# Kernel optimization log

Hardware: AMD Instinct MI355X
Metric: run time of the kernel (lower is better)

## Reference

```python
import jax, jax.numpy as jnp
import numpy as np

N_USER = 100000
N_ITEM = 50000
N = N_USER + N_ITEM  # 150000 nodes
D = 64               # embedding_size
L = 3                # num_layers
E = 2000000          # edges
B = 8192             # batch of (user, item_p, item_n) triples
INT_W, POP_W, TIDE_W = 0.1, 0.1, 0.2


def setup_inputs() -> dict:
    key = jax.random.key(0)
    ks = jax.random.split(key, 10)
    stdv = 1.0 / np.sqrt(D)
    emb_int = jax.random.uniform(ks[0], (N, D), minval=-stdv, maxval=stdv, dtype=jnp.float32)
    emb_pop = jax.random.uniform(ks[1], (N, D), minval=-stdv, maxval=stdv, dtype=jnp.float32)
    q = jax.random.uniform(ks[2], (N_ITEM,), dtype=jnp.float32)
    b = jax.random.uniform(ks[3], (N_ITEM,), dtype=jnp.float32)
    user = jax.random.randint(ks[4], (B, 1), 0, N_USER)
    item_p = jax.random.randint(ks[5], (B, 1), 0, N_ITEM)
    item_n = jax.random.randint(ks[6], (B, 1), 0, N_ITEM)
    mask = jax.random.randint(ks[7], (B, 1), 0, 2).astype(bool)
    edge_src = jax.random.randint(ks[8], (E,), 0, N)
    edge_dst = jax.random.randint(ks[9], (E,), 0, N)
    return {"emb_int": emb_int, "emb_pop": emb_pop, "q": q, "b": b,
            "user": user, "item_p": item_p, "item_n": item_n, "mask": mask,
            "edge_src": edge_src, "edge_dst": edge_dst}


def reference(emb_int, emb_pop, q, b, user, item_p, item_n, mask, edge_src, edge_dst):
    # --- LightGCN symmetric normalization coefficients (per edge) ---
    ones = jnp.ones(edge_src.shape, emb_int.dtype)
    deg_out = jax.ops.segment_sum(ones, edge_src, num_segments=N)
    deg_in = jax.ops.segment_sum(ones, edge_dst, num_segments=N)
    norm = (jax.lax.rsqrt(jnp.maximum(deg_out, 1.0))[edge_src]
            * jax.lax.rsqrt(jnp.maximum(deg_in, 1.0))[edge_dst])  # [E]

    def propagate(e0):
        # L layers of LGConv (gather-scale-scatter), mean over layer outputs incl. layer 0.
        # Dropout is identity in eval mode (training=False).
        acc, h = e0, e0
        for _ in range(L):
            h = jax.ops.segment_sum(h[edge_src] * norm[:, None], edge_dst, num_segments=N)
            acc = acc + h
        return acc / (L + 1)

    f_int = propagate(emb_int)  # [N, D]
    f_pop = propagate(emb_pop)  # [N, D]

    ip = item_p + N_USER  # item node ids
    inn = item_n + N_USER
    u_i, u_p = f_int[user], f_pop[user]          # [B, 1, D]
    pi_i, pi_p = f_int[ip], f_pop[ip]
    ni_i, ni_p = f_int[inn], f_pop[inn]

    p_score_int = jnp.sum(u_i * pi_i, axis=2)    # [B, 1]
    n_score_int = jnp.sum(u_i * ni_i, axis=2)
    p_score_pop = jnp.sum(u_p * pi_p, axis=2)
    n_score_pop = jnp.sum(u_p * ni_p, axis=2)
    p_score_total = p_score_int + p_score_pop
    n_score_total = n_score_int + n_score_pop

    mf = mask.astype(p_score_int.dtype)
    nmf = (~mask).astype(p_score_int.dtype)

    def mask_bpr(p, n, m):
        return -jnp.mean(m * jax.nn.log_sigmoid(p - n))

    def bpr(p, n):
        return -jnp.mean(jax.nn.log_sigmoid(p - n))

    loss_int = mask_bpr(p_score_int, n_score_int, mf)
    loss_pop = mask_bpr(n_score_pop, p_score_pop, mf) - mask_bpr(p_score_pop, n_score_pop, nmf)

    pop_p = jax.nn.softplus(q[item_p]) + jax.nn.softplus(b[item_p])  # [B, 1]
    pop_n = jax.nn.softplus(q[item_n]) + jax.nn.softplus(b[item_n])
    loss_tide = bpr(jnp.tanh(pop_p) * p_score_total, jnp.tanh(pop_n) * n_score_total)

    return INT_W * loss_int + POP_W * loss_pop + TIDE_W * loss_tide
```

## Files before the change

### kernel.cpp

```cpp
#include <hip/hip_runtime.h>
#include <hip/hip_bf16.h>
#include <math.h>

#define N_USER 100000
#define N_ITEM 50000
#define NNODE  150000
#define DIM    64
#define NEDGE  2000000
#define BSZ    8192
#define NTGT   (3*BSZ)
#define CB     586
#define NB     512
#define CH     ((NEDGE + NB - 1)/NB)
#define LBLK   2048
#define PREPB  (NNODE*32/256)
#define CAP    5120
#define BSLACK 772

typedef float v2f __attribute__((ext_vector_type(2)));
typedef unsigned v4u __attribute__((ext_vector_type(4)));

__device__ __forceinline__ float logsigf(float x){
    return fminf(x, 0.f) - log1pf(expf(-fabsf(x)));
}
__device__ __forceinline__ float softplusf(float x){
    return fmaxf(x, 0.f) + log1pf(expf(-fabsf(x)));
}
__device__ __forceinline__ v2f fp8x2_to_f32(unsigned short u){
    return __builtin_amdgcn_cvt_pk_f32_fp8((int)u, false);
}
__device__ __forceinline__ unsigned short f32_to_fp8x2(float a, float b){
    return (unsigned short)__builtin_amdgcn_cvt_pk_fp8_f32(a, b, 0, false);
}
__device__ __forceinline__ unsigned rfl(unsigned v){
    return (unsigned)__builtin_amdgcn_readfirstlane((int)v);
}
__device__ __forceinline__ v4u nt4(const unsigned* p){
    return __builtin_nontemporal_load((const v4u*)p);
}
__device__ __forceinline__ unsigned umin2(unsigned a, unsigned b){ return a<b ? a : b; }

__device__ __forceinline__ void scanCB(unsigned* arr, unsigned* tmp){
    int t = threadIdx.x;
    int base = 3*t;
    unsigned a0=0,a1=0,a2=0;
    if(base   < CB) a0 = arr[base];
    if(base+1 < CB) a1 = arr[base+1];
    if(base+2 < CB) a2 = arr[base+2];
    unsigned s = a0+a1+a2;
    tmp[t]=s; __syncthreads();
    for(int off=1; off<256; off<<=1){
        unsigned v = (t>=off)? tmp[t-off] : 0u;
        __syncthreads();
        tmp[t] += v;
        __syncthreads();
    }
    unsigned excl = tmp[t]-s;
    if(base   < CB) arr[base]   = excl;
    if(base+1 < CB) arr[base+1] = excl+a0;
    if(base+2 < CB) arr[base+2] = excl+a0+a1;
    __syncthreads();
}

__global__ __launch_bounds__(256) void k_hist(const int* __restrict__ src, const int* __restrict__ dst,
                       unsigned* __restrict__ histD, unsigned* __restrict__ histS,
                       const unsigned char* __restrict__ mask8, unsigned* __restrict__ mflag){
    if(blockIdx.x == NB){
        __shared__ int any;
        if(threadIdx.x==0) any=0;
        __syncthreads();
        for(int i=threadIdx.x;i<BSZ;i+=256){ if((i&3) && mask8[i]) any=1; }
        __syncthreads();
        if(threadIdx.x==0) *mflag = (any!=0) ? 1u : 0u;
        return;
    }
    __shared__ unsigned hD[CB], hS[CB];
    for(int i=threadIdx.x;i<CB;i+=256){ hD[i]=0; hS[i]=0; }
    __syncthreads();
    int lo = blockIdx.x*CH, hi = min(lo+CH, NEDGE);
    for(int e=lo+threadIdx.x; e<hi; e+=256){
        atomicAdd(&hS[src[e]>>8],1u);
        atomicAdd(&hD[dst[e]>>8],1u);
    }
    __syncthreads();
    for(int i=threadIdx.x;i<CB;i+=256){
        histD[(size_t)blockIdx.x*CB + i]=hD[i];
        histS[(size_t)blockIdx.x*CB + i]=hS[i];
    }
}

__global__ __launch_bounds__(512) void k_colscan(unsigned* __restrict__ histD, unsigned* __restrict__ histS,
                          unsigned* __restrict__ ctD, unsigned* __restrict__ ctS){
    unsigned* hist = blockIdx.y ? histS : histD;
    unsigned* ct   = blockIdx.y ? ctS   : ctD;
    int b = blockIdx.x;
    __shared__ unsigned sh[512];
    unsigned v = hist[(size_t)threadIdx.x*CB + b];
    sh[threadIdx.x] = v;
    __syncthreads();
    for(int off=1; off<512; off<<=1){
        unsigned t = (threadIdx.x>=off)? sh[threadIdx.x-off] : 0u;
        __syncthreads();
        sh[threadIdx.x] += t;
        __syncthreads();
    }
    hist[(size_t)threadIdx.x*CB + b] = sh[threadIdx.x] - v;
    if(threadIdx.x==511) ct[b] = sh[511];
}

__global__ __launch_bounds__(1024) void k_bstart(const unsigned* __restrict__ ctD, const unsigned* __restrict__ ctS,
                         unsigned* __restrict__ bsD, unsigned* __restrict__ bsS){
    __shared__ unsigned sh[1024];
    unsigned v = (threadIdx.x<CB)? ctD[threadIdx.x] : 0u;
    sh[threadIdx.x]=v; __syncthreads();
    for(int off=1; off<1024; off<<=1){ unsigned t=(threadIdx.x>=off)?sh[threadIdx.x-off]:0u; __syncthreads(); sh[threadIdx.x]+=t; __syncthreads(); }
    if(threadIdx.x<CB) bsD[threadIdx.x]=sh[threadIdx.x]-v;
    if(threadIdx.x==CB-1) bsD[CB]=sh[threadIdx.x];
    __syncthreads();
    unsigned v2 = (threadIdx.x<CB)? ctS[threadIdx.x] : 0u;
    sh[threadIdx.x]=v2; __syncthreads();
    for(int off=1; off<1024; off<<=1){ unsigned t=(threadIdx.x>=off)?sh[threadIdx.x-off]:0u; __syncthreads(); sh[threadIdx.x]+=t; __syncthreads(); }
    if(threadIdx.x<CB) bsS[threadIdx.x]=sh[threadIdx.x]-v2;
    if(threadIdx.x==CB-1) bsS[CB]=sh[threadIdx.x];
}

__global__ __launch_bounds__(256) void k_scatter(const int* __restrict__ src, const int* __restrict__ dst,
                          const unsigned* __restrict__ histD, const unsigned* __restrict__ histS,
                          const unsigned* __restrict__ bsD, const unsigned* __restrict__ bsS,
                          unsigned* __restrict__ part, unsigned char* __restrict__ spart){
    __shared__ unsigned curD[CB], curS[CB];
    __shared__ unsigned lhD[CB], lhS[CB];
    __shared__ unsigned startD[CB], startS[CB];
    __shared__ unsigned tmp[256];
    __shared__ unsigned partl[CH];
    __shared__ unsigned short keyD[CH];
    __shared__ unsigned short keyS[CH];
    __shared__ unsigned char sl[CH];
    for(int i=threadIdx.x;i<CB;i+=256){
        curD[i]=bsD[i]+histD[(size_t)blockIdx.x*CB+i];
        curS[i]=bsS[i]+histS[(size_t)blockIdx.x*CB+i];
        lhD[i]=0; lhS[i]=0;
    }
    __syncthreads();
    int lo=blockIdx.x*CH, hi=min(lo+CH,NEDGE);
    int n = hi-lo;
    for(int e=lo+threadIdx.x;e<hi;e+=256){
        atomicAdd(&lhD[dst[e]>>8],1u);
        atomicAdd(&lhS[src[e]>>8],1u);
    }
    __syncthreads();
    scanCB(lhD, tmp);
    scanCB(lhS, tmp);
    for(int i=threadIdx.x;i<CB;i+=256){ startD[i]=lhD[i]; startS[i]=lhS[i]; }
    __syncthreads();
    for(int e=lo+threadIdx.x;e<hi;e+=256){
        int s=src[e], d=dst[e];
        unsigned bd=(unsigned)(d>>8);
        unsigned slot=atomicAdd(&lhD[bd],1u);
        partl[slot]=((unsigned)(d&255)<<18)|(unsigned)s;
        keyD[slot]=(unsigned short)bd;
        unsigned bs=(unsigned)(s>>8);
        unsigned sslot=atomicAdd(&lhS[bs],1u);
        sl[sslot]=(unsigned char)(s&255);
        keyS[sslot]=(unsigned short)bs;
    }
    __syncthreads();
    for(int k=threadIdx.x;k<n;k+=256){
        unsigned b=keyD[k];
        part[curD[b] + (unsigned)k - startD[b]] = partl[k];
    }
    for(int k=threadIdx.x;k<n;k+=256){
        unsigned b=keyS[k];
        spart[curS[b] + (unsigned)k - startS[b]] = sl[k];
    }
}

__global__ __launch_bounds__(256) void k_degO(const unsigned char* __restrict__ spart, const unsigned* __restrict__ bsS,
                       float* __restrict__ rsqO, float* __restrict__ sqd){
    __shared__ unsigned cnt[256];
    cnt[threadIdx.x]=0;
    __syncthreads();
    unsigned lo=bsS[blockIdx.x], hi=bsS[blockIdx.x+1];
    for(unsigned e=lo+threadIdx.x;e<hi;e+=256) atomicAdd(&cnt[spart[e]],1u);
    __syncthreads();
    int node=(blockIdx.x<<8)+(int)threadIdx.x;
    if(node<NNODE){
        float dv = fmaxf((float)cnt[threadIdx.x],1.f);
        rsqO[node]=rsqrtf(dv);
        sqd[node]=sqrtf(dv)*0.125f;
    }
}

__global__ __launch_bounds__(256) void k_prep(const float4* __restrict__ ei, const float4* __restrict__ ep,
                      const float* __restrict__ rsqO,
                      unsigned* __restrict__ hE32, unsigned* __restrict__ h1g, unsigned* __restrict__ h2g){
    if(blockIdx.x == PREPB){
        int t = threadIdx.x;
        if(t < 32) hE32[t] = 0u;
        else if(t < 64) h1g[t-32] = 0u;
        else if(t < 96) h2g[t-64] = 0u;
        return;
    }
    int idx = blockIdx.x*256 + threadIdx.x;
    int n = idx>>5, c = idx&31;
    float sc = 8.f*rsqO[n];
    float4 v;
    if(c<16) v = ei[(size_t)n*16 + c];
    else     v = ep[(size_t)n*16 + (c-16)];
    int d = __builtin_amdgcn_cvt_pk_fp8_f32(v.x*sc, v.y*sc, 0, false);
    d = __builtin_amdgcn_cvt_pk_fp8_f32(v.z*sc, v.w*sc, d, true);
    hE32[32 + (size_t)n*32 + c] = (unsigned)d;
}

__global__ __launch_bounds__(256) void k_csr(const unsigned* __restrict__ part, const unsigned* __restrict__ bsD,
                      const float* __restrict__ rsqO,
                      unsigned* __restrict__ rs, unsigned* __restrict__ degI,
                      unsigned* __restrict__ ec, float* __restrict__ srow, float* __restrict__ rsqI8){
    __shared__ unsigned cnt[256], cur[256], sh[256];
    __shared__ unsigned stR[256], exR[256];
    __shared__ unsigned partl[CAP];
    cnt[threadIdx.x]=0;
    __syncthreads();
    unsigned lo=bsD[blockIdx.x], hi=bsD[blockIdx.x+1];
    unsigned n = hi-lo;
    for(unsigned e=lo+threadIdx.x;e<hi;e+=256) atomicAdd(&cnt[part[e]>>18],1u);
    __syncthreads();
    unsigned c=cnt[threadIdx.x];
    unsigned r4=(c+3u)&~3u;
    sh[threadIdx.x]=c; __syncthreads();
    for(int o=1;o<256;o<<=1){ unsigned t=(threadIdx.x>=o)?sh[threadIdx.x-o]:0u; __syncthreads(); sh[threadIdx.x]+=t; __syncthreads(); }
    unsigned ex = sh[threadIdx.x]-c;
    __syncthreads();
    sh[threadIdx.x]=r4; __syncthreads();
    for(int o=1;o<256;o<<=1){ unsigned t=(threadIdx.x>=o)?sh[threadIdx.x-o]:0u; __syncthreads(); sh[threadIdx.x]+=t; __syncthreads(); }
    unsigned ex_r = sh[threadIdx.x]-r4;
    stR[threadIdx.x]=ex; exR[threadIdx.x]=ex_r;
    cur[threadIdx.x]=(n<=CAP)? ex : ex_r;
    unsigned lo_ec = ((lo+3u)&~3u) + (unsigned)BSLACK*blockIdx.x;
    int node=(blockIdx.x<<8)+(int)threadIdx.x;
    if(node<NNODE){
        degI[node]=r4; rs[node]=lo_ec+ex_r;
        float rI = rsqrtf(fmaxf((float)c,1.f));
        float rO = rsqO[node];
        srow[node]  = rI*rO;
        rsqI8[node] = rI*0.125f;
    }
    for(unsigned j=c;j<r4;++j) ec[lo_ec+ex_r+j]=0u;
    __syncthreads();
    if(n <= CAP){
        for(unsigned e=lo+threadIdx.x;e<hi;e+=256){
            unsigned p=part[e];
            unsigned slot=atomicAdd(&cur[p>>18],1u);
            partl[slot]=p;
        }
        __syncthreads();
        for(unsigned k=threadIdx.x;k<n;k+=256){
            unsigned p=partl[k];
            unsigned fb=p>>18;
            ec[lo_ec + exR[fb] + (k - stR[fb])] = ((p&0x3FFFFu)+1u)<<7;
        }
    } else {
        for(unsigned e=lo+threadIdx.x;e<hi;e+=256){
            unsigned p=part[e];
            unsigned pos=lo_ec+atomicAdd(&cur[p>>18],1u);
            ec[pos] = ((p&0x3FFFFu)+1u)<<7;
        }
    }
}

__device__ __forceinline__ void drain4(const char* __restrict__ hb,
                                       const unsigned* __restrict__ ec,
                                       unsigned s, unsigned c, unsigned &i, unsigned lane2,
                                       v2f &acc){
    for(; i+4<=c; i+=4){
        v4u e = nt4(&ec[s+i]);
        unsigned short u0=*(const unsigned short*)(hb+e.x+lane2);
        unsigned short u1=*(const unsigned short*)(hb+e.y+lane2);
        unsigned short u2=*(const unsigned short*)(hb+e.z+lane2);
        unsigned short u3=*(const unsigned short*)(hb+e.w+lane2);
        acc += fp8x2_to_f32(u0); acc += fp8x2_to_f32(u1);
        acc += fp8x2_to_f32(u2); acc += fp8x2_to_f32(u3);
    }
}

__global__ __launch_bounds__(256) void k_spmm_c(const unsigned short* __restrict__ hinb, unsigned short* __restrict__ houtb,
                                                const unsigned* __restrict__ rs, const unsigned* __restrict__ degI,
                                                const unsigned* __restrict__ ec, const float* __restrict__ srow){
    int wv = (blockIdx.x*256 + threadIdx.x) >> 6;
    int lane = threadIdx.x & 63;
    int r = 4*wv;
    if(r >= NNODE) return;
    unsigned s0=rfl(rs[r  ]), c0=rfl(degI[r  ]);
    unsigned s1=rfl(rs[r+1]), c1=rfl(degI[r+1]);
    unsigned s2=rfl(rs[r+2]), c2=rfl(degI[r+2]);
    unsigned s3=rfl(rs[r+3]), c3=rfl(degI[r+3]);
    const char* hb = (const char*)hinb;
    unsigned lane2 = ((unsigned)lane)*2u;
    v2f a0={0.f,0.f}, a1={0.f,0.f}, a2={0.f,0.f}, a3={0.f,0.f};
    unsigned m = umin2(umin2(c0,c1), umin2(c2,c3));
    v4u eA, eB, eC, eD;
    if(m){
        eA=nt4(&ec[s0]); eB=nt4(&ec[s1]); eC=nt4(&ec[s2]); eD=nt4(&ec[s3]);
    }
    for(unsigned i=0; i<m; i+=4){
        unsigned ip = (i+4<m) ? i+4 : 0u;
        v4u fA=nt4(&ec[s0+ip]), fB=nt4(&ec[s1+ip]), fC=nt4(&ec[s2+ip]), fD=nt4(&ec[s3+ip]);
        unsigned short u00=*(const unsigned short*)(hb+eA.x+lane2);
        unsigned short u01=*(const unsigned short*)(hb+eA.y+lane2);
        unsigned short u02=*(const unsigned short*)(hb+eA.z+lane2);
        unsigned short u03=*(const unsigned short*)(hb+eA.w+lane2);
        unsigned short u10=*(const unsigned short*)(hb+eB.x+lane2);
        unsigned short u11=*(const unsigned short*)(hb+eB.y+lane2);
        unsigned short u12=*(const unsigned short*)(hb+eB.z+lane2);
        unsigned short u13=*(const unsigned short*)(hb+eB.w+lane2);
        unsigned short u20=*(const unsigned short*)(hb+eC.x+lane2);
        unsigned short u21=*(const unsigned short*)(hb+eC.y+lane2);
        unsigned short u22=*(const unsigned short*)(hb+eC.z+lane2);
        unsigned short u23=*(const unsigned short*)(hb+eC.w+lane2);
        unsigned short u30=*(const unsigned short*)(hb+eD.x+lane2);
        unsigned short u31=*(const unsigned short*)(hb+eD.y+lane2);
        unsigned short u32v=*(const unsigned short*)(hb+eD.z+lane2);
        unsigned short u33=*(const unsigned short*)(hb+eD.w+lane2);
        a0 += fp8x2_to_f32(u00); a0 += fp8x2_to_f32(u01); a0 += fp8x2_to_f32(u02); a0 += fp8x2_to_f32(u03);
        a1 += fp8x2_to_f32(u10); a1 += fp8x2_to_f32(u11); a1 += fp8x2_to_f32(u12); a1 += fp8x2_to_f32(u13);
        a2 += fp8x2_to_f32(u20); a2 += fp8x2_to_f32(u21); a2 += fp8x2_to_f32(u22); a2 += fp8x2_to_f32(u23);
        a3 += fp8x2_to_f32(u30); a3 += fp8x2_to_f32(u31); a3 += fp8x2_to_f32(u32v); a3 += fp8x2_to_f32(u33);
        eA=fA; eB=fB; eC=fC; eD=fD;
    }
    unsigned i0=m,i1=m,i2=m,i3=m;
    drain4(hb, ec, s0, c0, i0, lane2, a0);
    drain4(hb, ec, s1, c1, i1, lane2, a1);
    drain4(hb, ec, s2, c2, i2, lane2, a2);
    drain4(hb, ec, s3, c3, i3, lane2, a3);
    float sc0=srow[r], sc1=srow[r+1], sc2=srow[r+2], sc3=srow[r+3];
    houtb[(size_t)(r+1)*64+lane] = f32_to_fp8x2(sc0*a0.x, sc0*a0.y);
    houtb[(size_t)(r+2)*64+lane] = f32_to_fp8x2(sc1*a1.x, sc1*a1.y);
    houtb[(size_t)(r+3)*64+lane] = f32_to_fp8x2(sc2*a2.x, sc2*a2.y);
    houtb[(size_t)(r+4)*64+lane] = f32_to_fp8x2(sc3*a3.x, sc3*a3.y);
}

__global__ __launch_bounds__(256) void k_spmm_t(const unsigned short* __restrict__ hinb, float2* __restrict__ h3,
                                                const unsigned* __restrict__ rs, const unsigned* __restrict__ degI,
                                                const unsigned* __restrict__ ec, const float* __restrict__ rsqI8,
                                                const int* __restrict__ user, const int* __restrict__ itp,
                                                const int* __restrict__ itn){
    int wv = (blockIdx.x*256 + threadIdx.x) >> 6;
    int lane = threadIdx.x & 63;
    int t0 = 2*wv, t1 = 2*wv+1;
    if(t0 >= NTGT) return;
    int sec0 = t0>>13, b0 = t0&(BSZ-1);
    int sec1 = t1>>13, b1 = t1&(BSZ-1);
    int n0 = (sec0==0) ? user[b0] : ((sec0==1) ? itp[b0]+N_USER : itn[b0]+N_USER);
    int n1 = (sec1==0) ? user[b1] : ((sec1==1) ? itp[b1]+N_USER : itn[b1]+N_USER);
    n0 = __builtin_amdgcn_readfirstlane(n0);
    n1 = __builtin_amdgcn_readfirstlane(n1);
    unsigned s0 = rfl(rs[n0]), c0 = rfl(degI[n0]);
    unsigned s1 = rfl(rs[n1]), c1 = rfl(degI[n1]);
    const char* hb = (const char*)hinb;
    unsigned lane2 = ((unsigned)lane)*2u;
    v2f a0={0.f,0.f}, a1={0.f,0.f};
    unsigned m = umin2(c0,c1);
    v4u eA, eB;
    if(m){ eA=nt4(&ec[s0]); eB=nt4(&ec[s1]); }
    for(unsigned i=0; i<m; i+=4){
        unsigned ip = (i+4<m) ? i+4 : 0u;
        v4u fA=nt4(&ec[s0+ip]), fB=nt4(&ec[s1+ip]);
        unsigned short u0=*(const unsigned short*)(hb+eA.x+lane2);
        unsigned short u1=*(const unsigned short*)(hb+eA.y+lane2);
        unsigned short u2=*(const unsigned short*)(hb+eA.z+lane2);
        unsigned short u3=*(const unsigned short*)(hb+eA.w+lane2);
        unsigned short u4=*(const unsigned short*)(hb+eB.x+lane2);
        unsigned short u5=*(const unsigned short*)(hb+eB.y+lane2);
        unsigned short u6=*(const unsigned short*)(hb+eB.z+lane2);
        unsigned short u7=*(const unsigned short*)(hb+eB.w+lane2);
        a0 += fp8x2_to_f32(u0); a0 += fp8x2_to_f32(u1); a0 += fp8x2_to_f32(u2); a0 += fp8x2_to_f32(u3);
        a1 += fp8x2_to_f32(u4); a1 += fp8x2_to_f32(u5); a1 += fp8x2_to_f32(u6); a1 += fp8x2_to_f32(u7);
        eA=fA; eB=fB;
    }
    unsigned i0=m, i1=m;
    drain4(hb, ec, s0, c0, i0, lane2, a0);
    drain4(hb, ec, s1, c1, i1, lane2, a1);
    float t0s = rsqI8[n0], t1s = rsqI8[n1];
    h3[(size_t)t0*64+lane] = make_float2(a0.x*t0s, a0.y*t0s);
    h3[(size_t)t1*64+lane] = make_float2(a1.x*t1s, a1.y*t1s);
}

__global__ __launch_bounds__(256) void k_scoreloss(const float2* __restrict__ ei, const float2* __restrict__ ep,
                        const unsigned short* __restrict__ h1C, const unsigned short* __restrict__ h2C,
                        const float2* __restrict__ h3,
                        const float* __restrict__ q, const float* __restrict__ bq,
                        const int* __restrict__ user, const int* __restrict__ item_p, const int* __restrict__ item_n,
                        const void* __restrict__ mask, const unsigned* __restrict__ mflag,
                        const float* __restrict__ sqd,
                        float4* __restrict__ partial){
    int t = blockIdx.x*256 + threadIdx.x;
    int b = t >> 6, l = t & 63;
    int wv = threadIdx.x >> 6;
    __shared__ float4 wsum[4];
    int nu = user[b];
    int np = item_p[b] + N_USER;
    int nn = item_n[b] + N_USER;

    float2 e0u, e0p, e0n;
    if(l < 32){
        e0u = ei[(size_t)nu*32 + l]; e0p = ei[(size_t)np*32 + l]; e0n = ei[(size_t)nn*32 + l];
    } else {
        e0u = ep[(size_t)nu*32 + (l-32)]; e0p = ep[(size_t)np*32 + (l-32)]; e0n = ep[(size_t)nn*32 + (l-32)];
    }
    v2f h1u = fp8x2_to_f32(h1C[(size_t)(nu+1)*64 + l]);
    v2f h1p = fp8x2_to_f32(h1C[(size_t)(np+1)*64 + l]);
    v2f h1n = fp8x2_to_f32(h1C[(size_t)(nn+1)*64 + l]);
    v2f h2u = fp8x2_to_f32(h2C[(size_t)(nu+1)*64 + l]);
    v2f h2p = fp8x2_to_f32(h2C[(size_t)(np+1)*64 + l]);
    v2f h2n = fp8x2_to_f32(h2C[(size_t)(nn+1)*64 + l]);
    float2 h3u = h3[(size_t)b*64 + l];
    float2 h3p = h3[(size_t)(BSZ   + b)*64 + l];
    float2 h3n = h3[(size_t)(2*BSZ + b)*64 + l];

    float squ = sqd[nu], sqp = sqd[np], sqn = sqd[nn];

    float fux = e0u.x + squ*(h1u.x + h2u.x) + h3u.x, fuy = e0u.y + squ*(h1u.y + h2u.y) + h3u.y;
    float fpx = e0p.x + sqp*(h1p.x + h2p.x) + h3p.x, fpy = e0p.y + sqp*(h1p.y + h2p.y) + h3p.y;
    float fnx = e0n.x + sqn*(h1n.x + h2n.x) + h3n.x, fny = e0n.y + sqn*(h1n.y + h2n.y) + h3n.y;

    float dp = fux*fpx + fuy*fpy;
    float dn = fux*fnx + fuy*fny;
    for(int off=16; off; off>>=1){ dp += __shfl_down(dp,off,32); dn += __shfl_down(dn,off,32); }
    float pi  = __shfl(dp, 0, 64) * (1.f/16.f);
    float ni  = __shfl(dn, 0, 64) * (1.f/16.f);
    float pp  = __shfl(dp, 32, 64) * (1.f/16.f);
    float npp = __shfl(dn, 32, 64) * (1.f/16.f);
    if(l == 0){
        bool bytes = (*mflag)!=0;
        float mf = bytes ? (((const unsigned char*)mask)[b]?1.f:0.f)
                         : (((const int*)mask)[b]?1.f:0.f);
        float nmf = 1.f-mf;
        float a0 = mf  * logsigf(pi-ni);
        float a1 = mf  * logsigf(npp-pp);
        float a2 = nmf * logsigf(pp-npp);
        int ip=item_p[b], in_=item_n[b];
        float popp = softplusf(q[ip]) + softplusf(bq[ip]);
        float popn = softplusf(q[in_]) + softplusf(bq[in_]);
        float a3 = logsigf(tanhf(popp)*(pi+pp) - tanhf(popn)*(ni+npp));
        wsum[wv] = make_float4(a0,a1,a2,a3);
    }
    __syncthreads();
    if(threadIdx.x == 0){
        float4 s0=wsum[0], s1=wsum[1], s2=wsum[2], s3=wsum[3];
        partial[blockIdx.x] = make_float4(s0.x+s1.x+s2.x+s3.x, s0.y+s1.y+s2.y+s3.y,
                                          s0.z+s1.z+s2.z+s3.z, s0.w+s1.w+s2.w+s3.w);
    }
}

__global__ __launch_bounds__(256) void k_lossfin(const float4* __restrict__ partial, float* __restrict__ out){
    __shared__ float4 sh[256];
    float4 s = make_float4(0,0,0,0);
    for(int i=threadIdx.x; i<LBLK; i+=256){
        float4 v = partial[i];
        s.x+=v.x; s.y+=v.y; s.z+=v.z; s.w+=v.w;
    }
    sh[threadIdx.x]=s;
    __syncthreads();
    for(int off=128; off; off>>=1){
        if(threadIdx.x < off){
            float4 a=sh[threadIdx.x], b2=sh[threadIdx.x+off];
            sh[threadIdx.x]=make_float4(a.x+b2.x,a.y+b2.y,a.z+b2.z,a.w+b2.w);
        }
        __syncthreads();
    }
    if(threadIdx.x==0){
        const float invB = 1.f/(float)BSZ;
        float4 t = sh[0];
        float loss_int  = -t.x*invB;
        float loss_pop  = -t.y*invB + t.z*invB;
        float loss_tide = -t.w*invB;
        out[0] = 0.1f*loss_int + 0.1f*loss_pop + 0.2f*loss_tide;
    }
}

extern "C" void kernel_launch(void* const* d_in, const int* in_sizes, int n_in,
                              void* d_out, int out_size, void* d_ws, size_t ws_size,
                              hipStream_t stream){
    const float* emb_int = (const float*)d_in[0];
    const float* emb_pop = (const float*)d_in[1];
    const float* q    = (const float*)d_in[2];
    const float* bq   = (const float*)d_in[3];
    const int* user   = (const int*)d_in[4];
    const int* item_p = (const int*)d_in[5];
    const int* item_n = (const int*)d_in[6];
    const void* mask  = d_in[7];
    const int* esrc   = (const int*)d_in[8];
    const int* edst   = (const int*)d_in[9];

    char* ws = (char*)d_ws;
    size_t o = 0;
    auto take = [&](size_t bytes)->char*{ char* p = ws + o; o = (o + bytes + 255) & ~(size_t)255; return p; };
    unsigned* histD = (unsigned*)take((size_t)NB*CB*4);
    unsigned* histS = (unsigned*)take((size_t)NB*CB*4);
    unsigned* ctD   = (unsigned*)take((size_t)CB*4);
    unsigned* ctS   = (unsigned*)take((size_t)CB*4);
    unsigned* bsD   = (unsigned*)take((size_t)(CB+1)*4);
    unsigned* bsS   = (unsigned*)take((size_t)(CB+1)*4);
    unsigned* part  = (unsigned*)take((size_t)NEDGE*4);
    unsigned char* spart = (unsigned char*)take((size_t)NEDGE);
    float*    rsqO  = (float*)take((size_t)NNODE*4);
    float*    sqd   = (float*)take((size_t)NNODE*4);
    unsigned* rs    = (unsigned*)take((size_t)NNODE*4);
    unsigned* degI  = (unsigned*)take((size_t)NNODE*4);
    unsigned* ec    = (unsigned*)take((size_t)(NEDGE + BSLACK*CB + 16)*4);
    float*    srow  = (float*)take((size_t)NNODE*4);
    float*    rsqI8 = (float*)take((size_t)NNODE*4);
    unsigned short* hEb  = (unsigned short*)take((size_t)(NNODE+1)*64*2);
    unsigned short* h1Cb = (unsigned short*)take((size_t)(NNODE+1)*64*2);
    unsigned short* h2Cb = (unsigned short*)take((size_t)(NNODE+1)*64*2);
    float2*   h3    = (float2*)take((size_t)NTGT*64*8);
    float4*   partial = (float4*)take((size_t)LBLK*16);
    unsigned* mflag = (unsigned*)take(256);
    (void)ws_size; (void)in_sizes; (void)n_in; (void)out_size;

    k_hist<<<NB+1,256,0,stream>>>(esrc, edst, histD, histS,
                                  (const unsigned char*)mask, mflag);
    k_colscan<<<dim3(CB,2),512,0,stream>>>(histD, histS, ctD, ctS);
    k_bstart<<<1,1024,0,stream>>>(ctD, ctS, bsD, bsS);
    k_scatter<<<NB,256,0,stream>>>(esrc, edst, histD, histS, bsD, bsS, part, spart);
    k_degO<<<CB,256,0,stream>>>(spart, bsS, rsqO, sqd);
    k_csr<<<CB,256,0,stream>>>(part, bsD, rsqO, rs, degI, ec, srow, rsqI8);
    k_prep<<<PREPB+1,256,0,stream>>>((const float4*)emb_int, (const float4*)emb_pop, rsqO,
                                     (unsigned*)hEb, (unsigned*)h1Cb, (unsigned*)h2Cb);

    const int spB = ((NNODE/4)*64 + 255)/256;
    k_spmm_c<<<spB,256,0,stream>>>(hEb,  h1Cb, rs, degI, ec, srow);
    k_spmm_c<<<spB,256,0,stream>>>(h1Cb, h2Cb, rs, degI, ec, srow);
    k_spmm_t<<<((NTGT/2)*64 + 255)/256,256,0,stream>>>(h2Cb, h3, rs, degI, ec, rsqI8,
                                                 user, item_p, item_n);
    k_scoreloss<<<LBLK,256,0,stream>>>((const float2*)emb_int, (const float2*)emb_pop,
                                       h1Cb, h2Cb, h3, q, bq, user, item_p, item_n,
                                       mask, mflag, sqd, partial);
    k_lossfin<<<1,256,0,stream>>>(partial, (float*)d_out);
}
```

Measured before the change: 323.9 us.

## Fuse target-row SpMM into score/loss kernel and widen hist/scatter blocks to 512

Removes the separate k_spmm_t launch and its h3 intermediate buffer. The third-layer aggregation for the user, positive and negative item rows is now computed inside k_scoreloss, one wave per triple gathering three neighbor lists at once. This saves a launch and the h3 write and read-back, at the cost of losing the software prefetch of edge indices and possibly lowering occupancy in the loss kernel. Separately, k_hist and k_scatter move from 256 to 512 threads per block, with a matching 512-wide local scan.

```diff
diff --git a/kernel.cpp b/kernel.cpp
--- a/kernel.cpp
+++ b/kernel.cpp
@@ -62,28 +62,48 @@
     __syncthreads();
 }
 
-__global__ __launch_bounds__(256) void k_hist(const int* __restrict__ src, const int* __restrict__ dst,
+__device__ __forceinline__ void scanCB512(unsigned* arr, unsigned* tmp){
+    int t = threadIdx.x;
+    int base = 2*t;
+    unsigned a0=0,a1=0;
+    if(base   < CB) a0 = arr[base];
+    if(base+1 < CB) a1 = arr[base+1];
+    unsigned s = a0+a1;
+    tmp[t]=s; __syncthreads();
+    for(int off=1; off<512; off<<=1){
+        unsigned v = (t>=off)? tmp[t-off] : 0u;
+        __syncthreads();
+        tmp[t] += v;
+        __syncthreads();
+    }
+    unsigned excl = tmp[t]-s;
+    if(base   < CB) arr[base]   = excl;
+    if(base+1 < CB) arr[base+1] = excl+a0;
+    __syncthreads();
+}
+
+__global__ __launch_bounds__(512) void k_hist(const int* __restrict__ src, const int* __restrict__ dst,
                        unsigned* __restrict__ histD, unsigned* __restrict__ histS,
                        const unsigned char* __restrict__ mask8, unsigned* __restrict__ mflag){
     if(blockIdx.x == NB){
         __shared__ int any;
         if(threadIdx.x==0) any=0;
         __syncthreads();
-        for(int i=threadIdx.x;i<BSZ;i+=256){ if((i&3) && mask8[i]) any=1; }
+        for(int i=threadIdx.x;i<BSZ;i+=512){ if((i&3) && mask8[i]) any=1; }
         __syncthreads();
         if(threadIdx.x==0) *mflag = (any!=0) ? 1u : 0u;
         return;
     }
     __shared__ unsigned hD[CB], hS[CB];
-    for(int i=threadIdx.x;i<CB;i+=256){ hD[i]=0; hS[i]=0; }
+    for(int i=threadIdx.x;i<CB;i+=512){ hD[i]=0; hS[i]=0; }
     __syncthreads();
     int lo = blockIdx.x*CH, hi = min(lo+CH, NEDGE);
-    for(int e=lo+threadIdx.x; e<hi; e+=256){
+    for(int e=lo+threadIdx.x; e<hi; e+=512){
         atomicAdd(&hS[src[e]>>8],1u);
         atomicAdd(&hD[dst[e]>>8],1u);
     }
     __syncthreads();
-    for(int i=threadIdx.x;i<CB;i+=256){
+    for(int i=threadIdx.x;i<CB;i+=512){
         histD[(size_t)blockIdx.x*CB + i]=hD[i];
         histS[(size_t)blockIdx.x*CB + i]=hS[i];
     }
@@ -124,19 +144,19 @@
     if(threadIdx.x==CB-1) bsS[CB]=sh[threadIdx.x];
 }
 
-__global__ __launch_bounds__(256) void k_scatter(const int* __restrict__ src, const int* __restrict__ dst,
+__global__ __launch_bounds__(512) void k_scatter(const int* __restrict__ src, const int* __restrict__ dst,
                           const unsigned* __restrict__ histD, const unsigned* __restrict__ histS,
                           const unsigned* __restrict__ bsD, const unsigned* __restrict__ bsS,
                           unsigned* __restrict__ part, unsigned char* __restrict__ spart){
     __shared__ unsigned curD[CB], curS[CB];
     __shared__ unsigned lhD[CB], lhS[CB];
     __shared__ unsigned startD[CB], startS[CB];
-    __shared__ unsigned tmp[256];
+    __shared__ unsigned tmp[512];
     __shared__ unsigned partl[CH];
     __shared__ unsigned short keyD[CH];
     __shared__ unsigned short keyS[CH];
     __shared__ unsigned char sl[CH];
-    for(int i=threadIdx.x;i<CB;i+=256){
+    for(int i=threadIdx.x;i<CB;i+=512){
         curD[i]=bsD[i]+histD[(size_t)blockIdx.x*CB+i];
         curS[i]=bsS[i]+histS[(size_t)blockIdx.x*CB+i];
         lhD[i]=0; lhS[i]=0;
@@ -144,16 +164,16 @@
     __syncthreads();
     int lo=blockIdx.x*CH, hi=min(lo+CH,NEDGE);
     int n = hi-lo;
-    for(int e=lo+threadIdx.x;e<hi;e+=256){
+    for(int e=lo+threadIdx.x;e<hi;e+=512){
         atomicAdd(&lhD[dst[e]>>8],1u);
         atomicAdd(&lhS[src[e]>>8],1u);
     }
     __syncthreads();
-    scanCB(lhD, tmp);
-    scanCB(lhS, tmp);
-    for(int i=threadIdx.x;i<CB;i+=256){ startD[i]=lhD[i]; startS[i]=lhS[i]; }
-    __syncthreads();
-    for(int e=lo+threadIdx.x;e<hi;e+=256){
+    scanCB512(lhD, tmp);
+    scanCB512(lhS, tmp);
+    for(int i=threadIdx.x;i<CB;i+=512){ startD[i]=lhD[i]; startS[i]=lhS[i]; }
+    __syncthreads();
+    for(int e=lo+threadIdx.x;e<hi;e+=512){
         int s=src[e], d=dst[e];
         unsigned bd=(unsigned)(d>>8);
         unsigned slot=atomicAdd(&lhD[bd],1u);
@@ -165,11 +185,11 @@
         keyS[sslot]=(unsigned short)bs;
     }
     __syncthreads();
-    for(int k=threadIdx.x;k<n;k+=256){
+    for(int k=threadIdx.x;k<n;k+=512){
         unsigned b=keyD[k];
         part[curD[b] + (unsigned)k - startD[b]] = partl[k];
     }
-    for(int k=threadIdx.x;k<n;k+=256){
+    for(int k=threadIdx.x;k<n;k+=512){
         unsigned b=keyS[k];
         spart[curS[b] + (unsigned)k - startS[b]] = sl[k];
     }
@@ -339,55 +359,10 @@
     houtb[(size_t)(r+4)*64+lane] = f32_to_fp8x2(sc3*a3.x, sc3*a3.y);
 }
 
-__global__ __launch_bounds__(256) void k_spmm_t(const unsigned short* __restrict__ hinb, float2* __restrict__ h3,
-                                                const unsigned* __restrict__ rs, const unsigned* __restrict__ degI,
-                                                const unsigned* __restrict__ ec, const float* __restrict__ rsqI8,
-                                                const int* __restrict__ user, const int* __restrict__ itp,
-                                                const int* __restrict__ itn){
-    int wv = (blockIdx.x*256 + threadIdx.x) >> 6;
-    int lane = threadIdx.x & 63;
-    int t0 = 2*wv, t1 = 2*wv+1;
-    if(t0 >= NTGT) return;
-    int sec0 = t0>>13, b0 = t0&(BSZ-1);
-    int sec1 = t1>>13, b1 = t1&(BSZ-1);
-    int n0 = (sec0==0) ? user[b0] : ((sec0==1) ? itp[b0]+N_USER : itn[b0]+N_USER);
-    int n1 = (sec1==0) ? user[b1] : ((sec1==1) ? itp[b1]+N_USER : itn[b1]+N_USER);
-    n0 = __builtin_amdgcn_readfirstlane(n0);
-    n1 = __builtin_amdgcn_readfirstlane(n1);
-    unsigned s0 = rfl(rs[n0]), c0 = rfl(degI[n0]);
-    unsigned s1 = rfl(rs[n1]), c1 = rfl(degI[n1]);
-    const char* hb = (const char*)hinb;
-    unsigned lane2 = ((unsigned)lane)*2u;
-    v2f a0={0.f,0.f}, a1={0.f,0.f};
-    unsigned m = umin2(c0,c1);
-    v4u eA, eB;
-    if(m){ eA=nt4(&ec[s0]); eB=nt4(&ec[s1]); }
-    for(unsigned i=0; i<m; i+=4){
-        unsigned ip = (i+4<m) ? i+4 : 0u;
-        v4u fA=nt4(&ec[s0+ip]), fB=nt4(&ec[s1+ip]);
-        unsigned short u0=*(const unsigned short*)(hb+eA.x+lane2);
-        unsigned short u1=*(const unsigned short*)(hb+eA.y+lane2);
-        unsigned short u2=*(const unsigned short*)(hb+eA.z+lane2);
-        unsigned short u3=*(const unsigned short*)(hb+eA.w+lane2);
-        unsigned short u4=*(const unsigned short*)(hb+eB.x+lane2);
-        unsigned short u5=*(const unsigned short*)(hb+eB.y+lane2);
-        unsigned short u6=*(const unsigned short*)(hb+eB.z+lane2);
-        unsigned short u7=*(const unsigned short*)(hb+eB.w+lane2);
-        a0 += fp8x2_to_f32(u0); a0 += fp8x2_to_f32(u1); a0 += fp8x2_to_f32(u2); a0 += fp8x2_to_f32(u3);
-        a1 += fp8x2_to_f32(u4); a1 += fp8x2_to_f32(u5); a1 += fp8x2_to_f32(u6); a1 += fp8x2_to_f32(u7);
-        eA=fA; eB=fB;
-    }
-    unsigned i0=m, i1=m;
-    drain4(hb, ec, s0, c0, i0, lane2, a0);
-    drain4(hb, ec, s1, c1, i1, lane2, a1);
-    float t0s = rsqI8[n0], t1s = rsqI8[n1];
-    h3[(size_t)t0*64+lane] = make_float2(a0.x*t0s, a0.y*t0s);
-    h3[(size_t)t1*64+lane] = make_float2(a1.x*t1s, a1.y*t1s);
-}
-
 __global__ __launch_bounds__(256) void k_scoreloss(const float2* __restrict__ ei, const float2* __restrict__ ep,
                         const unsigned short* __restrict__ h1C, const unsigned short* __restrict__ h2C,
-                        const float2* __restrict__ h3,
+                        const unsigned* __restrict__ rs, const unsigned* __restrict__ degI,
+                        const unsigned* __restrict__ ec, const float* __restrict__ rsqI8,
                         const float* __restrict__ q, const float* __restrict__ bq,
                         const int* __restrict__ user, const int* __restrict__ item_p, const int* __restrict__ item_n,
                         const void* __restrict__ mask, const unsigned* __restrict__ mflag,
@@ -397,9 +372,43 @@
     int b = t >> 6, l = t & 63;
     int wv = threadIdx.x >> 6;
     __shared__ float4 wsum[4];
-    int nu = user[b];
-    int np = item_p[b] + N_USER;
-    int nn = item_n[b] + N_USER;
+    int nu = __builtin_amdgcn_readfirstlane(user[b]);
+    int np = __builtin_amdgcn_readfirstlane(item_p[b]) + N_USER;
+    int nn = __builtin_amdgcn_readfirstlane(item_n[b]) + N_USER;
+
+    unsigned s0 = rfl(rs[nu]), c0 = rfl(degI[nu]);
+    unsigned s1 = rfl(rs[np]), c1 = rfl(degI[np]);
+    unsigned s2 = rfl(rs[nn]), c2 = rfl(degI[nn]);
+    const char* hb = (const char*)h2C;
+    unsigned lane2 = ((unsigned)l)*2u;
+    v2f g0={0.f,0.f}, g1={0.f,0.f}, g2={0.f,0.f};
+    unsigned m = umin2(umin2(c0,c1), c2);
+    for(unsigned i=0; i<m; i+=4){
+        v4u eA=nt4(&ec[s0+i]), eB=nt4(&ec[s1+i]), eC=nt4(&ec[s2+i]);
+        unsigned short u0=*(const unsigned short*)(hb+eA.x+lane2);
+        unsigned short u1=*(const unsigned short*)(hb+eA.y+lane2);
+        unsigned short u2=*(const unsigned short*)(hb+eA.z+lane2);
+        unsigned short u3=*(const unsigned short*)(hb+eA.w+lane2);
+        unsigned short u4=*(const unsigned short*)(hb+eB.x+lane2);
+        unsigned short u5=*(const unsigned short*)(hb+eB.y+lane2);
+        unsigned short u6=*(const unsigned short*)(hb+eB.z+lane2);
+        unsigned short u7=*(const unsigned short*)(hb+eB.w+lane2);
+        unsigned short u8=*(const unsigned short*)(hb+eC.x+lane2);
+        unsigned short u9=*(const unsigned short*)(hb+eC.y+lane2);
+        unsigned short ua=*(const unsigned short*)(hb+eC.z+lane2);
+        unsigned short ub=*(const unsigned short*)(hb+eC.w+lane2);
+        g0 += fp8x2_to_f32(u0); g0 += fp8x2_to_f32(u1); g0 += fp8x2_to_f32(u2); g0 += fp8x2_to_f32(u3);
+        g1 += fp8x2_to_f32(u4); g1 += fp8x2_to_f32(u5); g1 += fp8x2_to_f32(u6); g1 += fp8x2_to_f32(u7);
+        g2 += fp8x2_to_f32(u8); g2 += fp8x2_to_f32(u9); g2 += fp8x2_to_f32(ua); g2 += fp8x2_to_f32(ub);
+    }
+    unsigned i0=m, i1=m, i2=m;
+    drain4(hb, ec, s0, c0, i0, lane2, g0);
+    drain4(hb, ec, s1, c1, i1, lane2, g1);
+    drain4(hb, ec, s2, c2, i2, lane2, g2);
+    float t0s = rsqI8[nu], t1s = rsqI8[np], t2s = rsqI8[nn];
+    float2 h3u = make_float2(g0.x*t0s, g0.y*t0s);
+    float2 h3p = make_float2(g1.x*t1s, g1.y*t1s);
+    float2 h3n = make_float2(g2.x*t2s, g2.y*t2s);
 
     float2 e0u, e0p, e0n;
     if(l < 32){
@@ -413,9 +422,6 @@
     v2f h2u = fp8x2_to_f32(h2C[(size_t)(nu+1)*64 + l]);
     v2f h2p = fp8x2_to_f32(h2C[(size_t)(np+1)*64 + l]);
     v2f h2n = fp8x2_to_f32(h2C[(size_t)(nn+1)*64 + l]);
-    float2 h3u = h3[(size_t)b*64 + l];
-    float2 h3p = h3[(size_t)(BSZ   + b)*64 + l];
-    float2 h3n = h3[(size_t)(2*BSZ + b)*64 + l];
 
     float squ = sqd[nu], sqp = sqd[np], sqn = sqd[nn];
 
@@ -446,9 +452,9 @@
     }
     __syncthreads();
     if(threadIdx.x == 0){
-        float4 s0=wsum[0], s1=wsum[1], s2=wsum[2], s3=wsum[3];
-        partial[blockIdx.x] = make_float4(s0.x+s1.x+s2.x+s3.x, s0.y+s1.y+s2.y+s3.y,
-                                          s0.z+s1.z+s2.z+s3.z, s0.w+s1.w+s2.w+s3.w);
+        float4 s0v=wsum[0], s1v=wsum[1], s2v=wsum[2], s3v=wsum[3];
+        partial[blockIdx.x] = make_float4(s0v.x+s1v.x+s2v.x+s3v.x, s0v.y+s1v.y+s2v.y+s3v.y,
+                                          s0v.z+s1v.z+s2v.z+s3v.z, s0v.w+s1v.w+s2v.w+s3v.w);
     }
 }
 
@@ -513,16 +519,15 @@
     unsigned short* hEb  = (unsigned short*)take((size_t)(NNODE+1)*64*2);
     unsigned short* h1Cb = (unsigned short*)take((size_t)(NNODE+1)*64*2);
     unsigned short* h2Cb = (unsigned short*)take((size_t)(NNODE+1)*64*2);
-    float2*   h3    = (float2*)take((size_t)NTGT*64*8);
     float4*   partial = (float4*)take((size_t)LBLK*16);
     unsigned* mflag = (unsigned*)take(256);
     (void)ws_size; (void)in_sizes; (void)n_in; (void)out_size;
 
-    k_hist<<<NB+1,256,0,stream>>>(esrc, edst, histD, histS,
+    k_hist<<<NB+1,512,0,stream>>>(esrc, edst, histD, histS,
                                   (const unsigned char*)mask, mflag);
     k_colscan<<<dim3(CB,2),512,0,stream>>>(histD, histS, ctD, ctS);
     k_bstart<<<1,1024,0,stream>>>(ctD, ctS, bsD, bsS);
-    k_scatter<<<NB,256,0,stream>>>(esrc, edst, histD, histS, bsD, bsS, part, spart);
+    k_scatter<<<NB,512,0,stream>>>(esrc, edst, histD, histS, bsD, bsS, part, spart);
     k_degO<<<CB,256,0,stream>>>(spart, bsS, rsqO, sqd);
     k_csr<<<CB,256,0,stream>>>(part, bsD, rsqO, rs, degI, ec, srow, rsqI8);
     k_prep<<<PREPB+1,256,0,stream>>>((const float4*)emb_int, (const float4*)emb_pop, rsqO,
@@ -531,10 +536,9 @@
     const int spB = ((NNODE/4)*64 + 255)/256;
     k_spmm_c<<<spB,256,0,stream>>>(hEb,  h1Cb, rs, degI, ec, srow);
     k_spmm_c<<<spB,256,0,stream>>>(h1Cb, h2Cb, rs, degI, ec, srow);
-    k_spmm_t<<<((NTGT/2)*64 + 255)/256,256,0,stream>>>(h2Cb, h3, rs, degI, ec, rsqI8,
-                                                 user, item_p, item_n);
     k_scoreloss<<<LBLK,256,0,stream>>>((const float2*)emb_int, (const float2*)emb_pop,
-                                       h1Cb, h2Cb, h3, q, bq, user, item_p, item_n,
+                                       h1Cb, h2Cb, rs, degI, ec, rsqI8,
+                                       q, bq, user, item_p, item_n,
                                        mask, mflag, sqd, partial);
     k_lossfin<<<1,256,0,stream>>>(partial, (float*)d_out);
 }
```

Result: faster. 304.7 us (-5.9%).
